# Performance work log

Hardware: AMD Instinct MI355X
Metric: run time of the kernel (lower is better)

## Reference

```python
import jax, jax.numpy as jnp
import numpy as np

HID = 256
FC1_OUT = 256


def setup_inputs() -> dict:
    key = jax.random.key(0)
    k1, k2, k3, k4, k5 = jax.random.split(key, 5)
    B, S = 64, 4096
    trg = jax.random.normal(k1, (B, S, HID), dtype=jnp.float32)
    src = jax.random.normal(k2, (B, 128, HID), dtype=jnp.float32)
    # fc_1: Linear(hid_dim, 256); fc_2: Linear(256, 1). PyTorch default init ~ U(-1/sqrt(fan_in), 1/sqrt(fan_in)).
    s1 = 1.0 / np.sqrt(HID)
    s2 = 1.0 / np.sqrt(FC1_OUT)
    W1 = jax.random.uniform(k3, (HID, FC1_OUT), minval=-s1, maxval=s1, dtype=jnp.float32)
    b1 = jnp.zeros((FC1_OUT,), dtype=jnp.float32)
    W2 = jax.random.uniform(k4, (FC1_OUT, 1), minval=-s2, maxval=s2, dtype=jnp.float32)
    b2 = jnp.zeros((1,), dtype=jnp.float32)
    return {"trg": trg, "src": src, "W1": W1, "b1": b1, "W2": W2, "b2": b2}


def reference(trg, src, W1, b1, W2, b2):
    # n_layers = 0: decoder layers are identity; src is unused.
    # Norm-weighted softmax pooling over the atom (sequence) dimension.
    norm = jnp.linalg.norm(trg, axis=2)            # [B, S]
    w = jax.nn.softmax(norm, axis=1)               # [B, S]
    pooled = jnp.einsum('bs,bsh->bh', w, trg)      # [B, hid] — replaces the double Python loop
    h = jax.nn.relu(pooled @ W1 + b1)              # dropout = identity at inference
    label = h @ W2 + b2                            # [B, 1]
    return label
```

## Files before the change

### kernel.cpp

```cpp
#include <hip/hip_runtime.h>
#include <math.h>

#define BATCH 64
#define SEQ   4096
#define HID   256
#define NBLK  32
#define ROWS_PER_BLK (SEQ / NBLK)
#define THREADS 256
#define NWAVE (THREADS / 64)
#define GSZ   16
#define NGRP  (THREADS / GSZ)
#define ITERS (ROWS_PER_BLK / NGRP)
#define VPL   (HID / (GSZ * 4))

__global__ __launch_bounds__(THREADS) void pool_pass(
        const float* __restrict__ trg,
        float* __restrict__ ws_m,
        float* __restrict__ ws_l,
        float* __restrict__ ws_p) {
    const int b     = blockIdx.x / NBLK;
    const int chunk = blockIdx.x % NBLK;
    const int tid   = threadIdx.x;
    const int wave  = tid >> 6;
    const int lane  = tid & 63;
    const int gid   = tid >> 4;
    const int sub   = tid & 15;
    const int gw    = gid & 3;

    const float* base = trg + ((size_t)b * SEQ + (size_t)chunk * ROWS_PER_BLK) * HID
                      + (size_t)gid * HID + sub * 4;

    float m = -INFINITY, l = 0.f;
    float4 acc[VPL];
    #pragma unroll
    for (int q = 0; q < VPL; ++q) acc[q] = make_float4(0.f, 0.f, 0.f, 0.f);

    float4 v0[VPL], v1[VPL];

    #define LOADV(dst, t)                                                     \
        {                                                                     \
            const float* rp_ = base + (size_t)(t) * (NGRP * HID);             \
            _Pragma("unroll")                                                 \
            for (int q = 0; q < VPL; ++q)                                     \
                dst[q] = *reinterpret_cast<const float4*>(rp_ + q * (GSZ*4)); \
        }

    #define PROCESS(v)                                                        \
        {                                                                     \
            float ss = 0.f;                                                   \
            _Pragma("unroll")                                                 \
            for (int q = 0; q < VPL; ++q)                                     \
                ss += v[q].x * v[q].x + v[q].y * v[q].y                       \
                    + v[q].z * v[q].z + v[q].w * v[q].w;                      \
            ss += __shfl_xor(ss, 1, 64);                                      \
            ss += __shfl_xor(ss, 2, 64);                                      \
            ss += __shfl_xor(ss, 4, 64);                                      \
            ss += __shfl_xor(ss, 8, 64);                                      \
            const float nrm = sqrtf(ss);                                      \
            if (nrm > m + 8.f) {                         \
                const float sc_ = __expf(m - nrm);                            \
                l *= sc_;                                                     \
                _Pragma("unroll")                                             \
                for (int q = 0; q < VPL; ++q) {                               \
                    acc[q].x *= sc_; acc[q].y *= sc_;                         \
                    acc[q].z *= sc_; acc[q].w *= sc_;                         \
                }                                                             \
                m = nrm;                                                      \
            }                                                                 \
            const float p = __expf(nrm - m);                      \
            l += p;                                                           \
            _Pragma("unroll")                                                 \
            for (int q = 0; q < VPL; ++q) {                                   \
                acc[q].x = fmaf(p, v[q].x, acc[q].x);                         \
                acc[q].y = fmaf(p, v[q].y, acc[q].y);                         \
                acc[q].z = fmaf(p, v[q].z, acc[q].z);                         \
                acc[q].w = fmaf(p, v[q].w, acc[q].w);                         \
            }                                                                 \
        }

    LOADV(v0, 0)
    #pragma unroll
    for (int t = 0; t < ITERS; t += 2) {
        LOADV(v1, t + 1)
        PROCESS(v0)
        if (t + 2 < ITERS) LOADV(v0, t + 2)
        PROCESS(v1)
    }
    #undef LOADV
    #undef PROCESS

    float m_w = m;
    m_w = fmaxf(m_w, __shfl_xor(m_w, 16, 64));
    m_w = fmaxf(m_w, __shfl_xor(m_w, 32, 64));
    const float sc = __expf(m - m_w);
    float l_w = l * sc;
    l_w += __shfl_xor(l_w, 16, 64);
    l_w += __shfl_xor(l_w, 32, 64);
    #pragma unroll
    for (int q = 0; q < VPL; ++q) {
        float4 a = acc[q];
        a.x *= sc; a.y *= sc; a.z *= sc; a.w *= sc;
        a.x += __shfl_xor(a.x, 16, 64);
        a.y += __shfl_xor(a.y, 16, 64);
        a.z += __shfl_xor(a.z, 16, 64);
        a.w += __shfl_xor(a.w, 16, 64);
        a.x += __shfl_xor(a.x, 32, 64);
        a.y += __shfl_xor(a.y, 32, 64);
        a.z += __shfl_xor(a.z, 32, 64);
        a.w += __shfl_xor(a.w, 32, 64);
        acc[q] = a;
    }

    float4 mine = acc[0];
    #pragma unroll
    for (int q = 1; q < VPL; ++q) if (gw == q) mine = acc[q];

    __shared__ float s_p[NWAVE][HID];
    __shared__ float s_m[NWAVE];
    __shared__ float s_l[NWAVE];
    *reinterpret_cast<float4*>(&s_p[wave][gw * 64 + sub * 4]) = mine;
    if (lane == 0) { s_m[wave] = m_w; s_l[wave] = l_w; }
    __syncthreads();

    const int j = tid;
    const float m_blk = fmaxf(fmaxf(s_m[0], s_m[1]), fmaxf(s_m[2], s_m[3]));
    const float e0 = __expf(s_m[0] - m_blk);
    const float e1 = __expf(s_m[1] - m_blk);
    const float e2 = __expf(s_m[2] - m_blk);
    const float e3 = __expf(s_m[3] - m_blk);
    const float pj = e0 * s_p[0][j] + e1 * s_p[1][j]
                   + e2 * s_p[2][j] + e3 * s_p[3][j];
    const int pidx = b * NBLK + chunk;
    ws_p[(size_t)pidx * HID + j] = pj;
    if (j == 0) {
        ws_m[pidx] = m_blk;
        ws_l[pidx] = e0 * s_l[0] + e1 * s_l[1] + e2 * s_l[2] + e3 * s_l[3];
    }
}

__global__ __launch_bounds__(THREADS) void finish_pass(
        const float* __restrict__ ws_m,
        const float* __restrict__ ws_l,
        const float* __restrict__ ws_p,
        const float* __restrict__ W1,
        const float* __restrict__ b1,
        const float* __restrict__ W2,
        const float* __restrict__ b2,
        float* __restrict__ out) {
    const int b = blockIdx.x;
    const int j = threadIdx.x;

    __shared__ float s_m[NBLK];
    __shared__ float s_l[NBLK];
    __shared__ float s_scale[NBLK];
    __shared__ float s_pooled[HID];
    __shared__ float s_red[NWAVE];

    if (j < NBLK) {
        s_m[j] = ws_m[b * NBLK + j];
        s_l[j] = ws_l[b * NBLK + j];
    }
    __syncthreads();

    float m = s_m[0];
    #pragma unroll
    for (int i = 1; i < NBLK; ++i) m = fmaxf(m, s_m[i]);
    if (j < NBLK) s_scale[j] = __expf(s_m[j] - m);
    __syncthreads();

    float l = 0.f, pj = 0.f;
    #pragma unroll 8
    for (int i = 0; i < NBLK; ++i) {
        l  = fmaf(s_l[i], s_scale[i], l);
        pj = fmaf(ws_p[(size_t)(b * NBLK + i) * HID + j], s_scale[i], pj);
    }
    s_pooled[j] = pj / l;
    __syncthreads();

    float h = b1[j];
    #pragma unroll 16
    for (int k = 0; k < HID; ++k)
        h = fmaf(s_pooled[k], W1[k * HID + j], h);
    h = fmaxf(h, 0.f);

    float v = h * W2[j];
    #pragma unroll
    for (int off = 32; off > 0; off >>= 1)
        v += __shfl_xor(v, off, 64);
    if ((j & 63) == 0) s_red[j >> 6] = v;
    __syncthreads();
    if (j == 0)
        out[b] = s_red[0] + s_red[1] + s_red[2] + s_red[3] + b2[0];
}

extern "C" void kernel_launch(void* const* d_in, const int* in_sizes, int n_in,
                              void* d_out, int out_size, void* d_ws, size_t ws_size,
                              hipStream_t stream) {
    const float* trg = (const float*)d_in[0];
    const float* W1  = (const float*)d_in[2];
    const float* b1  = (const float*)d_in[3];
    const float* W2  = (const float*)d_in[4];
    const float* b2  = (const float*)d_in[5];
    float* out = (float*)d_out;

    float* ws_m = (float*)d_ws;
    float* ws_l = ws_m + BATCH * NBLK;
    float* ws_p = ws_l + BATCH * NBLK;

    pool_pass<<<dim3(BATCH * NBLK), THREADS, 0, stream>>>(trg, ws_m, ws_l, ws_p);
    finish_pass<<<dim3(BATCH), THREADS, 0, stream>>>(ws_m, ws_l, ws_p,
                                                     W1, b1, W2, b2, out);
}
```

Baseline: 54.55 us.

## Halve pool blocks, use nontemporal vector loads, vectorize math, disable loop unroll

```diff
diff --git a/kernel.cpp b/kernel.cpp
--- a/kernel.cpp
+++ b/kernel.cpp
@@ -4,7 +4,7 @@
 #define BATCH 64
 #define SEQ   4096
 #define HID   256
-#define NBLK  32
+#define NBLK  16
 #define ROWS_PER_BLK (SEQ / NBLK)
 #define THREADS 256
 #define NWAVE (THREADS / 64)
@@ -12,6 +12,8 @@
 #define NGRP  (THREADS / GSZ)
 #define ITERS (ROWS_PER_BLK / NGRP)
 #define VPL   (HID / (GSZ * 4))
+
+typedef float f4 __attribute__((ext_vector_type(4)));
 
 __global__ __launch_bounds__(THREADS) void pool_pass(
         const float* __restrict__ trg,
@@ -31,27 +33,27 @@
                       + (size_t)gid * HID + sub * 4;
 
     float m = -INFINITY, l = 0.f;
-    float4 acc[VPL];
-    #pragma unroll
-    for (int q = 0; q < VPL; ++q) acc[q] = make_float4(0.f, 0.f, 0.f, 0.f);
-
-    float4 v0[VPL], v1[VPL];
+    f4 acc[VPL];
+    #pragma unroll
+    for (int q = 0; q < VPL; ++q) acc[q] = (f4)0.f;
+
+    f4 v0[VPL], v1[VPL];
 
     #define LOADV(dst, t)                                                     \
         {                                                                     \
             const float* rp_ = base + (size_t)(t) * (NGRP * HID);             \
             _Pragma("unroll")                                                 \
             for (int q = 0; q < VPL; ++q)                                     \
-                dst[q] = *reinterpret_cast<const float4*>(rp_ + q * (GSZ*4)); \
+                dst[q] = __builtin_nontemporal_load(                          \
+                    reinterpret_cast<const f4*>(rp_ + q * (GSZ * 4)));        \
         }
 
     #define PROCESS(v)                                                        \
         {                                                                     \
-            float ss = 0.f;                                                   \
+            f4 sq = v[0] * v[0];                                              \
             _Pragma("unroll")                                                 \
-            for (int q = 0; q < VPL; ++q)                                     \
-                ss += v[q].x * v[q].x + v[q].y * v[q].y                       \
-                    + v[q].z * v[q].z + v[q].w * v[q].w;                      \
+            for (int q = 1; q < VPL; ++q) sq += v[q] * v[q];                  \
+            float ss = sq.x + sq.y + sq.z + sq.w;                             \
             ss += __shfl_xor(ss, 1, 64);                                      \
             ss += __shfl_xor(ss, 2, 64);                                      \
             ss += __shfl_xor(ss, 4, 64);                                      \
@@ -61,25 +63,17 @@
                 const float sc_ = __expf(m - nrm);                            \
                 l *= sc_;                                                     \
                 _Pragma("unroll")                                             \
-                for (int q = 0; q < VPL; ++q) {                               \
-                    acc[q].x *= sc_; acc[q].y *= sc_;                         \
-                    acc[q].z *= sc_; acc[q].w *= sc_;                         \
-                }                                                             \
+                for (int q = 0; q < VPL; ++q) acc[q] *= sc_;                  \
                 m = nrm;                                                      \
             }                                                                 \
             const float p = __expf(nrm - m);                      \
             l += p;                                                           \
             _Pragma("unroll")                                                 \
-            for (int q = 0; q < VPL; ++q) {                                   \
-                acc[q].x = fmaf(p, v[q].x, acc[q].x);                         \
-                acc[q].y = fmaf(p, v[q].y, acc[q].y);                         \
-                acc[q].z = fmaf(p, v[q].z, acc[q].z);                         \
-                acc[q].w = fmaf(p, v[q].w, acc[q].w);                         \
-            }                                                                 \
+            for (int q = 0; q < VPL; ++q) acc[q] += p * v[q];                 \
         }
 
     LOADV(v0, 0)
-    #pragma unroll
+    #pragma unroll 1
     for (int t = 0; t < ITERS; t += 2) {
         LOADV(v1, t + 1)
         PROCESS(v0)
@@ -98,8 +92,7 @@
     l_w += __shfl_xor(l_w, 32, 64);
     #pragma unroll
     for (int q = 0; q < VPL; ++q) {
-        float4 a = acc[q];
-        a.x *= sc; a.y *= sc; a.z *= sc; a.w *= sc;
+        f4 a = acc[q] * sc;
         a.x += __shfl_xor(a.x, 16, 64);
         a.y += __shfl_xor(a.y, 16, 64);
         a.z += __shfl_xor(a.z, 16, 64);
@@ -111,14 +104,14 @@
         acc[q] = a;
     }
 
-    float4 mine = acc[0];
+    f4 mine = acc[0];
     #pragma unroll
     for (int q = 1; q < VPL; ++q) if (gw == q) mine = acc[q];
 
     __shared__ float s_p[NWAVE][HID];
     __shared__ float s_m[NWAVE];
     __shared__ float s_l[NWAVE];
-    *reinterpret_cast<float4*>(&s_p[wave][gw * 64 + sub * 4]) = mine;
+    *reinterpret_cast<f4*>(&s_p[wave][gw * 64 + sub * 4]) = mine;
     if (lane == 0) { s_m[wave] = m_w; s_l[wave] = l_w; }
     __syncthreads();
 
```

Measured after the change: 51.62 us. 5.4% less time.
